# Performance work log

Hardware: AMD Instinct MI355X
Metric: run time of the kernel (lower is better)

The kernel has to match this reference:

```python
import jax, jax.numpy as jnp
import numpy as np

DIM = 1024
STATE = 64
HEADS = 8
EXPAND = 2
INNER = DIM * EXPAND          # 2048
HEAD_DIM = INNER // HEADS     # 256
KERNEL = 4
B, L = 2, 2048
EPS = 1e-5


def setup_inputs() -> dict:
    key = jax.random.key(0)
    ks = jax.random.split(key, 12)
    s = 0.02
    return {
        "input_tensor": jax.random.normal(ks[0], (B, L, DIM), jnp.float32),
        "Wx": jax.random.normal(ks[1], (INNER, DIM), jnp.float32) * s,
        "Wz": jax.random.normal(ks[2], (INNER, DIM), jnp.float32) * s,
        "conv_w": jax.random.normal(ks[3], (INNER, 1, KERNEL), jnp.float32) * s,
        "conv_b": jnp.zeros((INNER,), jnp.float32),
        "Wb": jax.random.normal(ks[4], (HEADS * STATE, INNER), jnp.float32) * s,
        "Wc": jax.random.normal(ks[5], (HEADS * STATE, INNER), jnp.float32) * s,
        "Wdt": jax.random.normal(ks[6], (HEADS, INNER), jnp.float32) * s,
        "b_dt": jnp.zeros((HEADS,), jnp.float32),
        "log_a": jnp.log(jnp.full((HEADS,), 0.5, jnp.float32)),
        "d_param": jnp.ones((HEADS,), jnp.float32),
        "gn_w": jnp.ones((INNER,), jnp.float32),
        "gn_b": jnp.zeros((INNER,), jnp.float32),
        "Wout": jax.random.normal(ks[7], (DIM, INNER), jnp.float32) * s,
    }


def _causal_conv(x, conv_w, conv_b):
    # x: (B, L, INNER); depthwise conv, kernel 4, left-pad 3 (causal)
    x_pad = jnp.pad(x, ((0, 0), (KERNEL - 1, 0), (0, 0)))
    w = conv_w[:, 0, :]  # (INNER, K)
    y = sum(x_pad[:, k:k + x.shape[1], :] * w[:, k] for k in range(KERNEL))
    return y + conv_b


def _ssd_scan(x, b, c, dt, a):
    # x: (B,L,H,P) b,c: (B,L,H,N) dt: (B,L,H) a: (H,)
    state0 = jnp.zeros((x.shape[0], HEADS, STATE, HEAD_DIM), x.dtype)

    def step(state, inp):
        x_t, b_t, c_t, dt_t = inp  # (B,H,P),(B,H,N),(B,H,N),(B,H)
        decay = jnp.exp(dt_t * a)[..., None, None]          # (B,H,1,1)
        b_bar = (dt_t[..., None] * b_t)                      # (B,H,N)
        state = decay * state + b_bar[..., None] * x_t[:, :, None, :]
        y_t = jnp.einsum("bhn,bhnp->bhp", c_t, state)
        return state, y_t

    xs = (x.transpose(1, 0, 2, 3), b.transpose(1, 0, 2, 3),
          c.transpose(1, 0, 2, 3), dt.transpose(1, 0, 2))
    _, ys = jax.lax.scan(step, state0, xs)  # ys: (L,B,H,P)
    return ys.transpose(1, 0, 2, 3)


def reference(input_tensor, Wx, Wz, conv_w, conv_b, Wb, Wc, Wdt, b_dt,
              log_a, d_param, gn_w, gn_b, Wout):
    bsz, seq, _ = input_tensor.shape
    x = input_tensor @ Wx.T               # (B,L,INNER)
    z = input_tensor @ Wz.T
    x = _causal_conv(x, conv_w, conv_b)
    x = jax.nn.silu(x)
    b = (x @ Wb.T).reshape(bsz, seq, HEADS, STATE)
    c = (x @ Wc.T).reshape(bsz, seq, HEADS, STATE)
    dt = jax.nn.softplus(x @ Wdt.T + b_dt)  # (B,L,H)
    xh = x.reshape(bsz, seq, HEADS, HEAD_DIM)
    a = -jnp.exp(log_a)
    y = _ssd_scan(xh, b, c, dt, a)
    y = y + d_param[None, None, :, None] * xh
    # GroupNorm(HEADS, INNER) applied on (B, C, L): normalize per (batch, group)
    # over (channels-in-group, sequence)
    yg = y  # (B, L, H, P) -- groups are contiguous channel blocks = heads
    mean = yg.mean(axis=(1, 3), keepdims=True)
    var = yg.var(axis=(1, 3), keepdims=True)
    yn = (yg - mean) / jnp.sqrt(var + EPS)
    yn = yn * gn_w.reshape(1, 1, HEADS, HEAD_DIM) + gn_b.reshape(1, 1, HEADS, HEAD_DIM)
    yn = yn.reshape(bsz, seq, INNER)
    out = yn * jax.nn.silu(z)
    return out @ Wout.T
```

## Files before the change

kernel.cpp:

```cpp
#include <hip/hip_runtime.h>
#include <math.h>

#define DIM_   1024
#define STATE_ 64
#define HEADS_ 8
#define INNER_ 2048
#define HDIM_  256
#define B_     2
#define L_     2048
#define M_     (B_*L_)
#define EPS_   1e-5f
#define Q_     64
#define NC_    (L_/Q_)
#define NCHUNK_ (B_*HEADS_*NC_)
#define BCS_   1024
#define XZS_   4096

typedef _Float16 f16;
typedef __attribute__((ext_vector_type(8))) _Float16 half8;
typedef __attribute__((ext_vector_type(4))) _Float16 half4;
typedef __attribute__((ext_vector_type(4))) float    f32x4;

__device__ __forceinline__ float siluf(float x) { return x / (1.f + expf(-x)); }

__device__ __forceinline__ void gload_lds16(const void* g, void* l) {
    __builtin_amdgcn_global_load_lds((const __attribute__((address_space(1))) void*)g,
                                     (__attribute__((address_space(3))) void*)l, 16, 0, 0);
}

__global__ __launch_bounds__(256) void cast_all(const float* __restrict__ in0,
                                                const float* __restrict__ Wx,
                                                const float* __restrict__ Wz,
                                                const float* __restrict__ Wb,
                                                const float* __restrict__ Wc,
                                                const float* __restrict__ Wout,
                                                f16* __restrict__ input_h,
                                                f16* __restrict__ wxz_h,
                                                f16* __restrict__ wbc_h,
                                                f16* __restrict__ wout_h) {
    int i = blockIdx.x * 256 + threadIdx.x;
    const float* src; f16* dst; int off;
    if      (i < 1048576) { src = in0;  dst = input_h;            off = i; }
    else if (i < 1572864) { src = Wx;   dst = wxz_h;              off = i - 1048576; }
    else if (i < 2097152) { src = Wz;   dst = wxz_h + 2097152;    off = i - 1572864; }
    else if (i < 2359296) { src = Wb;   dst = wbc_h;              off = i - 2097152; }
    else if (i < 2621440) { src = Wc;   dst = wbc_h + 1048576;    off = i - 2359296; }
    else                  { src = Wout; dst = wout_h;             off = i - 2621440; }
    float4 v = *(const float4*)&src[(size_t)off * 4];
    half4 o;
    o[0] = (f16)v.x; o[1] = (f16)v.y; o[2] = (f16)v.z; o[3] = (f16)v.w;
    *(half4*)&dst[(size_t)off * 4] = o;
}

template<int BN, bool OUTF16>
__global__ __launch_bounds__(256) void hgemm(const f16* __restrict__ A,
                                             const f16* __restrict__ W,
                                             void* __restrict__ Cout,
                                             int K, int N) {
    constexpr int N_FR = BN / 32;
    constexpr int NITER = (128 + BN) / 64;
    __shared__ f16 sA[128 * 32];
    __shared__ f16 sW[BN * 32];
    const int tid  = threadIdx.x;
    const int wid  = tid >> 6;
    const int lane = tid & 63;
    const int bm = blockIdx.y * 128;
    const int bn = blockIdx.x * BN;
    const int wr = wid >> 1, wc = wid & 1;
    const int r  = lane & 15, kg = lane >> 4;

    const f16* gsrc[NITER];
    f16* ldst[NITER];
#pragma unroll
    for (int i = 0; i < NITER; ++i) {
        int slot = tid + i * 256;
        if (slot < 512) {
            int row = slot >> 2;
            int kgv = ((slot & 3) ^ ((row >> 1) & 3)) * 8;
            gsrc[i] = A + (size_t)(bm + row) * K + kgv;
        } else {
            int row = (slot - 512) >> 2;
            int kgv = ((slot & 3) ^ ((row >> 1) & 3)) * 8;
            gsrc[i] = W + (size_t)(bn + row) * K + kgv;
        }
        int slot0 = (tid & ~63) + i * 256;
        ldst[i] = (slot0 < 512) ? &sA[slot0 * 8] : &sW[(slot0 - 512) * 8];
    }

    int aoff[4], boff[N_FR];
#pragma unroll
    for (int m = 0; m < 4; ++m) {
        int arow = wr * 64 + m * 16 + r;
        aoff[m] = arow * 32 + ((kg ^ ((arow >> 1) & 3)) << 3);
    }
#pragma unroll
    for (int n = 0; n < N_FR; ++n) {
        int wrow = wc * (BN / 2) + n * 16 + r;
        boff[n] = wrow * 32 + ((kg ^ ((wrow >> 1) & 3)) << 3);
    }

    f32x4 acc[4][N_FR];
#pragma unroll
    for (int m = 0; m < 4; ++m)
#pragma unroll
        for (int n = 0; n < N_FR; ++n) acc[m][n] = (f32x4)0.f;

    for (int k0 = 0; k0 < K; k0 += 32) {
#pragma unroll
        for (int i = 0; i < NITER; ++i) gload_lds16(gsrc[i] + k0, ldst[i]);
        __syncthreads();
        half8 av[4], bv[N_FR];
#pragma unroll
        for (int m = 0; m < 4; ++m) av[m] = *(const half8*)&sA[aoff[m]];
#pragma unroll
        for (int n = 0; n < N_FR; ++n) bv[n] = *(const half8*)&sW[boff[n]];
#pragma unroll
        for (int m = 0; m < 4; ++m)
#pragma unroll
            for (int n = 0; n < N_FR; ++n)
                acc[m][n] = __builtin_amdgcn_mfma_f32_16x16x32_f16(av[m], bv[n], acc[m][n], 0, 0, 0);
        __syncthreads();
    }

#pragma unroll
    for (int m = 0; m < 4; ++m)
#pragma unroll
        for (int n = 0; n < N_FR; ++n) {
            int row0o = bm + wr * 64 + m * 16 + kg * 4;
            int col   = bn + wc * (BN / 2) + n * 16 + r;
#pragma unroll
            for (int j = 0; j < 4; ++j) {
                if (OUTF16) ((f16*)Cout)[(size_t)(row0o + j) * N + col] = (f16)acc[m][n][j];
                else        ((float*)Cout)[(size_t)(row0o + j) * N + col] = acc[m][n][j];
            }
        }
}

__global__ __launch_bounds__(256) void conv_silu_dt(const f16* __restrict__ xz,
                                                    const float* __restrict__ cw,
                                                    const float* __restrict__ cb,
                                                    const float* __restrict__ Wdt,
                                                    const float* __restrict__ bdt,
                                                    f16* __restrict__ xc,
                                                    float* __restrict__ dtb) {
    __shared__ float sred[4][HEADS_];
    const int m = blockIdx.x;
    const int tid = threadIdx.x;
    const int c8 = tid * 8;
    const int t = m & (L_ - 1);
    float acc[8];
    float4 wv[8];
#pragma unroll
    for (int j = 0; j < 8; ++j) { acc[j] = cb[c8 + j]; wv[j] = *(const float4*)&cw[(c8 + j) * 4]; }
#pragma unroll
    for (int k = 0; k < 4; ++k) {
        int tt = t - 3 + k;
        if (tt >= 0) {
            half8 xv = *(const half8*)&xz[(size_t)(m - 3 + k) * XZS_ + c8];
#pragma unroll
            for (int j = 0; j < 8; ++j) acc[j] += (float)xv[j] * ((const float*)&wv[j])[k];
        }
    }
    float xf[8];
    half8 o;
#pragma unroll
    for (int j = 0; j < 8; ++j) { xf[j] = siluf(acc[j]); o[j] = (f16)xf[j]; }
    *(half8*)&xc[(size_t)m * INNER_ + c8] = o;

    float p[HEADS_];
#pragma unroll
    for (int h = 0; h < HEADS_; ++h) {
        float4 w0 = *(const float4*)&Wdt[h * INNER_ + c8];
        float4 w1 = *(const float4*)&Wdt[h * INNER_ + c8 + 4];
        p[h] = xf[0]*w0.x + xf[1]*w0.y + xf[2]*w0.z + xf[3]*w0.w
             + xf[4]*w1.x + xf[5]*w1.y + xf[6]*w1.z + xf[7]*w1.w;
    }
#pragma unroll
    for (int h = 0; h < HEADS_; ++h)
#pragma unroll
        for (int off = 32; off > 0; off >>= 1)
            p[h] += __shfl_down(p[h], off, 64);
    if ((tid & 63) == 0) {
#pragma unroll
        for (int h = 0; h < HEADS_; ++h) sred[tid >> 6][h] = p[h];
    }
    __syncthreads();
    if (tid < 32) {
        float v = sred[tid >> 3][tid & 7];
        v += __shfl_down(v, 16, 32);
        v += __shfl_down(v, 8, 32);
        if (tid < 8) {
            float s = v + bdt[tid];
            dtb[(size_t)m * HEADS_ + tid] = (s > 20.f) ? s : log1pf(expf(s));
        }
    }
}

__global__ __launch_bounds__(256) void ssd_phase1(const float* __restrict__ bc,
                                                  const float* __restrict__ dtb,
                                                  const float* __restrict__ log_a,
                                                  float* __restrict__ pbuf,
                                                  float* __restrict__ eAbuf,
                                                  float* __restrict__ wbuf,
                                                  float* __restrict__ cdecay) {
    __shared__ float sBt[STATE_][Q_+1];
    __shared__ float sCt[STATE_][Q_+1];
    __shared__ float sA[Q_];
    __shared__ float sDt[Q_];
    const int tid = threadIdx.x;
    const int chunk = blockIdx.x;
    const int bh = chunk / NC_;
    const int ck = chunk - bh * NC_;
    const int b = bh >> 3, h = bh & 7;
    const int m0 = b * L_ + ck * Q_;

    if (tid < 64) {
        float dt = dtb[(size_t)(m0 + tid) * HEADS_ + h];
        float a = -expf(log_a[h]);
        float x = dt * a;
#pragma unroll
        for (int off = 1; off < 64; off <<= 1) {
            float v = __shfl_up(x, off, 64);
            if (tid >= off) x += v;
        }
        float Alast = __shfl(x, 63, 64);
        sA[tid] = x;
        sDt[tid] = dt;
        eAbuf[(size_t)(m0 + tid) * HEADS_ + h] = expf(x);
        wbuf[(size_t)chunk * Q_ + tid] = expf(Alast - x) * dt;
        if (tid == 0) cdecay[chunk] = expf(Alast);
    }
#pragma unroll
    for (int l = 0; l < 4; ++l) {
        int q = tid + l * 256;
        int s = q >> 4;
        int n0 = (q & 15) * 4;
        float4 bv = *(const float4*)&bc[(size_t)(m0+s)*BCS_ + h*STATE_ + n0];
        float4 cv = *(const float4*)&bc[(size_t)(m0+s)*BCS_ + 512 + h*STATE_ + n0];
        sBt[n0+0][s] = bv.x; sBt[n0+1][s] = bv.y; sBt[n0+2][s] = bv.z; sBt[n0+3][s] = bv.w;
        sCt[n0+0][s] = cv.x; sCt[n0+1][s] = cv.y; sCt[n0+2][s] = cv.z; sCt[n0+3][s] = cv.w;
    }
    __syncthreads();
    const int tx = tid & 15, ty = tid >> 4;
    float g[4][4];
#pragma unroll
    for (int i = 0; i < 4; ++i)
#pragma unroll
        for (int j = 0; j < 4; ++j) g[i][j] = 0.f;
    for (int n = 0; n < STATE_; ++n) {
        float cv[4], bv[4];
#pragma unroll
        for (int i = 0; i < 4; ++i) cv[i] = sCt[n][ty*4+i];
#pragma unroll
        for (int j = 0; j < 4; ++j) bv[j] = sBt[n][tx*4+j];
#pragma unroll
        for (int i = 0; i < 4; ++i)
#pragma unroll
            for (int j = 0; j < 4; ++j) g[i][j] += cv[i] * bv[j];
    }
#pragma unroll
    for (int i = 0; i < 4; ++i) {
        int t = ty*4 + i;
        float At = sA[t];
        float o[4];
#pragma unroll
        for (int j = 0; j < 4; ++j) {
            int s = tx*4 + j;
            o[j] = (t >= s) ? g[i][j] * expf(At - sA[s]) * sDt[s] : 0.f;
        }
        *(float4*)&pbuf[((size_t)chunk * Q_ + t) * Q_ + tx*4] = make_float4(o[0],o[1],o[2],o[3]);
    }
}

__global__ __launch_bounds__(256) void ssd_phase2(const float* __restrict__ bc,
                                                  const f16* __restrict__ xch,
                                                  const float* __restrict__ pbuf,
                                                  const float* __restrict__ wbuf,
                                                  float* __restrict__ ybuf,
                                                  float* __restrict__ sloc) {
    __shared__ float sPt[Q_][Q_+1];
    __shared__ float sBw[Q_][STATE_+1];
    __shared__ float sX[Q_][Q_+4];
    const int tid = threadIdx.x;
    const int chunk = blockIdx.x;
    const int bh = chunk / NC_;
    const int ck = chunk - bh * NC_;
    const int b = bh >> 3, h = bh & 7;
    const int m0 = b * L_ + ck * Q_;

#pragma unroll
    for (int l = 0; l < 4; ++l) {
        int q = tid + l * 256;
        int t = q >> 4;
        int s0 = (q & 15) * 4;
        float4 pv = *(const float4*)&pbuf[((size_t)chunk*Q_ + t)*Q_ + s0];
        sPt[s0+0][t] = pv.x; sPt[s0+1][t] = pv.y; sPt[s0+2][t] = pv.z; sPt[s0+3][t] = pv.w;
        int s = t;
        int n0 = s0;
        float ws = wbuf[(size_t)chunk * Q_ + s];
        float4 bv = *(const float4*)&bc[(size_t)(m0+s)*BCS_ + h*STATE_ + n0];
        sBw[s][n0+0] = bv.x * ws; sBw[s][n0+1] = bv.y * ws;
        sBw[s][n0+2] = bv.z * ws; sBw[s][n0+3] = bv.w * ws;
    }
    const int tx = tid & 15, ty = tid >> 4;
    for (int pt = 0; pt < 4; ++pt) {
        int p0 = pt * 64;
        __syncthreads();
#pragma unroll
        for (int l = 0; l < 2; ++l) {
            int q = tid + l * 256;
            int s = q >> 3;
            int pp = (q & 7) * 8;
            half8 xv = *(const half8*)&xch[(size_t)(m0+s)*INNER_ + h*HDIM_ + p0 + pp];
#pragma unroll
            for (int j = 0; j < 8; ++j) sX[s][pp+j] = (float)xv[j];
        }
        __syncthreads();
        float accY[4][4], accS[4][4];
#pragma unroll
        for (int i = 0; i < 4; ++i)
#pragma unroll
            for (int j = 0; j < 4; ++j) { accY[i][j] = 0.f; accS[i][j] = 0.f; }
        for (int s = 0; s < Q_; ++s) {
            float pv[4], bv[4];
#pragma unroll
            for (int i = 0; i < 4; ++i) { pv[i] = sPt[s][ty*4+i]; bv[i] = sBw[s][ty*4+i]; }
            float4 xv = *(const float4*)&sX[s][tx*4];
            float xq[4] = {xv.x, xv.y, xv.z, xv.w};
#pragma unroll
            for (int i = 0; i < 4; ++i)
#pragma unroll
                for (int j = 0; j < 4; ++j) {
                    accY[i][j] += pv[i] * xq[j];
                    accS[i][j] += bv[i] * xq[j];
                }
        }
#pragma unroll
        for (int i = 0; i < 4; ++i) {
            int t = ty*4 + i;
            *(float4*)&ybuf[(size_t)(m0+t)*INNER_ + h*HDIM_ + p0 + tx*4] =
                make_float4(accY[i][0], accY[i][1], accY[i][2], accY[i][3]);
            *(float4*)&sloc[((size_t)chunk*STATE_ + t)*HDIM_ + p0 + tx*4] =
                make_float4(accS[i][0], accS[i][1], accS[i][2], accS[i][3]);
        }
    }
}

__global__ __launch_bounds__(256) void chunk_scan_k(float* __restrict__ sloc,
                                                    const float* __restrict__ cdecay) {
    int bh = blockIdx.x >> 6;
    int el = (blockIdx.x & 63) * 256 + threadIdx.x;
    float s = 0.f;
    for (int c = 0; c < NC_; ++c) {
        size_t chunk = (size_t)bh * NC_ + c;
        float* ptr = sloc + chunk * (size_t)(STATE_*HDIM_) + el;
        float tmp = *ptr;
        *ptr = s;
        s = cdecay[chunk] * s + tmp;
    }
}

__global__ __launch_bounds__(256) void ssd_phase3(const float* __restrict__ bc,
                                                  const f16* __restrict__ xch,
                                                  const float* __restrict__ sloc,
                                                  const float* __restrict__ eAbuf,
                                                  const float* __restrict__ dparam,
                                                  float* __restrict__ ybuf,
                                                  float* __restrict__ gstats) {
    __shared__ float sCt[STATE_][Q_+1];
    __shared__ float sS[STATE_][Q_+4];
    __shared__ float red[512];
    const int tid = threadIdx.x;
    const int chunk = blockIdx.x;
    const int bh = chunk / NC_;
    const int ck = chunk - bh * NC_;
    const int b = bh >> 3, h = bh & 7;
    const int m0 = b * L_ + ck * Q_;

#pragma unroll
    for (int l = 0; l < 4; ++l) {
        int q = tid + l * 256;
        int t = q >> 4;
        int n0 = (q & 15) * 4;
        float4 cv = *(const float4*)&bc[(size_t)(m0+t)*BCS_ + 512 + h*STATE_ + n0];
        sCt[n0+0][t] = cv.x; sCt[n0+1][t] = cv.y; sCt[n0+2][t] = cv.z; sCt[n0+3][t] = cv.w;
    }
    const int tx = tid & 15, ty = tid >> 4;
    const float d = dparam[h];
    float lsum = 0.f, lsq = 0.f;
    for (int pt = 0; pt < 4; ++pt) {
        int p0 = pt * 64;
        __syncthreads();
#pragma unroll
        for (int l = 0; l < 4; ++l) {
            int q = tid + l * 256;
            int n = q >> 4;
            int pp = (q & 15) * 4;
            *(float4*)&sS[n][pp] = *(const float4*)&sloc[((size_t)chunk*STATE_ + n)*HDIM_ + p0 + pp];
        }
        __syncthreads();
        float acc[4][4];
#pragma unroll
        for (int i = 0; i < 4; ++i)
#pragma unroll
            for (int j = 0; j < 4; ++j) acc[i][j] = 0.f;
        for (int n = 0; n < STATE_; ++n) {
            float cv[4];
#pragma unroll
            for (int i = 0; i < 4; ++i) cv[i] = sCt[n][ty*4+i];
            float4 sv = *(const float4*)&sS[n][tx*4];
            float sq[4] = {sv.x, sv.y, sv.z, sv.w};
#pragma unroll
            for (int i = 0; i < 4; ++i)
#pragma unroll
                for (int j = 0; j < 4; ++j) acc[i][j] += cv[i] * sq[j];
        }
#pragma unroll
        for (int i = 0; i < 4; ++i) {
            int t = ty*4 + i;
            float eA = eAbuf[(size_t)(m0+t)*HEADS_ + h];
            size_t off = (size_t)(m0+t)*INNER_ + h*HDIM_ + p0 + tx*4;
            float4 yin = *(const float4*)&ybuf[off];
            half4 xv4 = *(const half4*)&xch[off];
            float4 o;
            o.x = yin.x + eA*acc[i][0] + d*(float)xv4[0];
            o.y = yin.y + eA*acc[i][1] + d*(float)xv4[1];
            o.z = yin.z + eA*acc[i][2] + d*(float)xv4[2];
            o.w = yin.w + eA*acc[i][3] + d*(float)xv4[3];
            *(float4*)&ybuf[off] = o;
            lsum += o.x + o.y + o.z + o.w;
            lsq  += o.x*o.x + o.y*o.y + o.z*o.z + o.w*o.w;
        }
    }
    __syncthreads();
    red[tid] = lsum; red[256+tid] = lsq;
    __syncthreads();
    for (int st = 128; st > 0; st >>= 1) {
        if (tid < st) { red[tid] += red[tid+st]; red[256+tid] += red[256+tid+st]; }
        __syncthreads();
    }
    if (tid == 0) {
        atomicAdd(&gstats[bh*2+0], red[0]);
        atomicAdd(&gstats[bh*2+1], red[256]);
    }
}

__global__ __launch_bounds__(256) void gn_gate_h(const float* __restrict__ ybuf,
                                                 const f16* __restrict__ xz,
                                                 const float* __restrict__ gstats,
                                                 const float* __restrict__ gnw,
                                                 const float* __restrict__ gnb,
                                                 f16* __restrict__ g) {
    int idx = blockIdx.x * 256 + threadIdx.x;
    int c8 = (idx & (INNER_/8 - 1)) * 8;
    int m = idx >> 8;
    int bh = (m >> 11) * HEADS_ + (c8 >> 8);
    const float cnt = (float)(L_ * HDIM_);
    float mean = gstats[bh*2] / cnt;
    float var  = gstats[bh*2+1] / cnt - mean*mean;
    float rstd = rsqrtf(var + EPS_);
    size_t off = (size_t)m * INNER_ + c8;
    float4 y0 = *(const float4*)&ybuf[off];
    float4 y1 = *(const float4*)&ybuf[off + 4];
    half8 zv = *(const half8*)&xz[(size_t)m * XZS_ + INNER_ + c8];
    float4 w0 = *(const float4*)&gnw[c8], w1 = *(const float4*)&gnw[c8+4];
    float4 b0 = *(const float4*)&gnb[c8], b1 = *(const float4*)&gnb[c8+4];
    float yn[8] = {y0.x, y0.y, y0.z, y0.w, y1.x, y1.y, y1.z, y1.w};
    float wv[8] = {w0.x, w0.y, w0.z, w0.w, w1.x, w1.y, w1.z, w1.w};
    float bv[8] = {b0.x, b0.y, b0.z, b0.w, b1.x, b1.y, b1.z, b1.w};
    half8 o;
#pragma unroll
    for (int j = 0; j < 8; ++j) {
        float v = (yn[j] - mean) * rstd * wv[j] + bv[j];
        o[j] = (f16)(v * siluf((float)zv[j]));
    }
    *(half8*)&g[off] = o;
}

extern "C" void kernel_launch(void* const* d_in, const int* in_sizes, int n_in,
                              void* d_out, int out_size, void* d_ws, size_t ws_size,
                              hipStream_t stream) {
    const float* input  = (const float*)d_in[0];
    const float* Wx     = (const float*)d_in[1];
    const float* Wz     = (const float*)d_in[2];
    const float* conv_w = (const float*)d_in[3];
    const float* conv_b = (const float*)d_in[4];
    const float* Wb     = (const float*)d_in[5];
    const float* Wc     = (const float*)d_in[6];
    const float* Wdt    = (const float*)d_in[7];
    const float* b_dt   = (const float*)d_in[8];
    const float* log_a  = (const float*)d_in[9];
    const float* d_par  = (const float*)d_in[10];
    const float* gn_w   = (const float*)d_in[11];
    const float* gn_b   = (const float*)d_in[12];
    const float* Wout   = (const float*)d_in[13];
    float* out = (float*)d_out;

    float* ws = (float*)d_ws;
    size_t off = 0;
    auto alloc = [&](size_t nfloats) { float* p = ws + off; off += (nfloats + 63) & ~(size_t)63; return p; };
    f16* input_h = (f16*)alloc((size_t)M_*DIM_/2);
    f16* wxz_h   = (f16*)alloc((size_t)XZS_*DIM_/2);
    f16* wbc_h   = (f16*)alloc((size_t)BCS_*INNER_/2);
    f16* wout_h  = (f16*)alloc((size_t)DIM_*INNER_/2);
    f16* xz_h    = (f16*)alloc((size_t)M_*XZS_/2);
    f16* xconv_h = (f16*)alloc((size_t)M_*INNER_/2);
    f16* gbuf_h  = (f16*)alloc((size_t)M_*INNER_/2);
    float* bcmat = alloc((size_t)M_*BCS_);
    float* dtb   = alloc((size_t)M_*HEADS_);
    float* eAb   = alloc((size_t)M_*HEADS_);
    float* wbuf  = alloc((size_t)NCHUNK_*Q_);
    float* ybuf  = alloc((size_t)M_*INNER_);
    float* pbuf  = alloc((size_t)NCHUNK_*Q_*Q_);
    float* sloc  = alloc((size_t)NCHUNK_*STATE_*HDIM_);
    float* cdec  = alloc((size_t)NCHUNK_);
    float* gstat = alloc((size_t)2*B_*HEADS_);

    dim3 blk(256);

    cast_all<<<12288, blk, 0, stream>>>(input, Wx, Wz, Wb, Wc, Wout,
                                        input_h, wxz_h, wbc_h, wout_h);
    hgemm<128,true><<<dim3(XZS_/128, M_/128), blk, 0, stream>>>(input_h, wxz_h, xz_h, DIM_, XZS_);
    conv_silu_dt<<<M_, blk, 0, stream>>>(xz_h, conv_w, conv_b, Wdt, b_dt, xconv_h, dtb);
    hgemm<64,false><<<dim3(BCS_/64, M_/128), blk, 0, stream>>>(xconv_h, wbc_h, bcmat, INNER_, BCS_);
    ssd_phase1<<<NCHUNK_, blk, 0, stream>>>(bcmat, dtb, log_a, pbuf, eAb, wbuf, cdec);
    ssd_phase2<<<NCHUNK_, blk, 0, stream>>>(bcmat, xconv_h, pbuf, wbuf, ybuf, sloc);
    chunk_scan_k<<<B_*HEADS_*64, blk, 0, stream>>>(sloc, cdec);
    hipMemsetAsync(gstat, 0, 2*B_*HEADS_*sizeof(float), stream);
    ssd_phase3<<<NCHUNK_, blk, 0, stream>>>(bcmat, xconv_h, sloc, eAb, d_par, ybuf, gstat);
    gn_gate_h<<<(M_*(INNER_/8))/256, blk, 0, stream>>>(ybuf, xz_h, gstat, gn_w, gn_b, gbuf_h);
    hgemm<64,false><<<dim3(DIM_/64, M_/128), blk, 0, stream>>>(gbuf_h, wout_h, out, INNER_, DIM_);
}
```

Measured before the change: 405.2 us.

## Move chunked SSD scan matmuls onto fp16 MFMA with transposed operands

Result: faster. 363.3 us (-10.4%).

```diff
diff --git a/kernel.cpp b/kernel.cpp
--- a/kernel.cpp
+++ b/kernel.cpp
@@ -196,15 +196,44 @@
     }
 }
 
-__global__ __launch_bounds__(256) void ssd_phase1(const float* __restrict__ bc,
+__global__ __launch_bounds__(256) void xpose_k(const f16* __restrict__ xc,
+                                               f16* __restrict__ xT) {
+    __shared__ f16 sT[64][72];
+    const int blk = blockIdx.x;
+    const int bh = blk >> 7;
+    const int rem = blk & 127;
+    const int tt = rem >> 2;
+    const int pt = rem & 3;
+    const int b = bh >> 3, h = bh & 7;
+    const int tid = threadIdx.x;
+#pragma unroll
+    for (int it = 0; it < 2; ++it) {
+        int q = tid + it * 256;
+        int tr = q >> 3;
+        int p0 = (q & 7) * 8;
+        half8 v = *(const half8*)&xc[(size_t)(b * L_ + tt * 64 + tr) * INNER_ + h * HDIM_ + pt * 64 + p0];
+        *(half8*)&sT[tr][p0] = v;
+    }
+    __syncthreads();
+#pragma unroll
+    for (int it = 0; it < 2; ++it) {
+        int q = tid + it * 256;
+        int pr = q >> 3;
+        int t0 = (q & 7) * 8;
+        half8 v;
+#pragma unroll
+        for (int j = 0; j < 8; ++j) v[j] = sT[t0 + j][pr];
+        *(half8*)&xT[((size_t)bh * HDIM_ + pt * 64 + pr) * L_ + tt * 64 + t0] = v;
+    }
+}
+
+__global__ __launch_bounds__(256) void ssd_phase1(const f16* __restrict__ bc,
                                                   const float* __restrict__ dtb,
                                                   const float* __restrict__ log_a,
-                                                  float* __restrict__ pbuf,
+                                                  f16* __restrict__ pbuf,
                                                   float* __restrict__ eAbuf,
                                                   float* __restrict__ wbuf,
                                                   float* __restrict__ cdecay) {
-    __shared__ float sBt[STATE_][Q_+1];
-    __shared__ float sCt[STATE_][Q_+1];
     __shared__ float sA[Q_];
     __shared__ float sDt[Q_];
     const int tid = threadIdx.x;
@@ -230,145 +259,137 @@
         wbuf[(size_t)chunk * Q_ + tid] = expf(Alast - x) * dt;
         if (tid == 0) cdecay[chunk] = expf(Alast);
     }
-#pragma unroll
-    for (int l = 0; l < 4; ++l) {
-        int q = tid + l * 256;
-        int s = q >> 4;
-        int n0 = (q & 15) * 4;
-        float4 bv = *(const float4*)&bc[(size_t)(m0+s)*BCS_ + h*STATE_ + n0];
-        float4 cv = *(const float4*)&bc[(size_t)(m0+s)*BCS_ + 512 + h*STATE_ + n0];
-        sBt[n0+0][s] = bv.x; sBt[n0+1][s] = bv.y; sBt[n0+2][s] = bv.z; sBt[n0+3][s] = bv.w;
-        sCt[n0+0][s] = cv.x; sCt[n0+1][s] = cv.y; sCt[n0+2][s] = cv.z; sCt[n0+3][s] = cv.w;
-    }
     __syncthreads();
-    const int tx = tid & 15, ty = tid >> 4;
-    float g[4][4];
-#pragma unroll
-    for (int i = 0; i < 4; ++i)
-#pragma unroll
-        for (int j = 0; j < 4; ++j) g[i][j] = 0.f;
-    for (int n = 0; n < STATE_; ++n) {
-        float cv[4], bv[4];
-#pragma unroll
-        for (int i = 0; i < 4; ++i) cv[i] = sCt[n][ty*4+i];
-#pragma unroll
-        for (int j = 0; j < 4; ++j) bv[j] = sBt[n][tx*4+j];
-#pragma unroll
-        for (int i = 0; i < 4; ++i)
-#pragma unroll
-            for (int j = 0; j < 4; ++j) g[i][j] += cv[i] * bv[j];
-    }
-#pragma unroll
-    for (int i = 0; i < 4; ++i) {
-        int t = ty*4 + i;
-        float At = sA[t];
-        float o[4];
+
+    const int w = tid >> 6, lane = tid & 63;
+    const int r = lane & 15, kg = lane >> 4;
+    const int ft = w;
+    const f16* Crow = bc + (size_t)(m0 + ft * 16 + r) * BCS_ + 512 + h * STATE_;
+    half8 a0 = *(const half8*)(Crow + kg * 8);
+    half8 a1 = *(const half8*)(Crow + 32 + kg * 8);
+#pragma unroll
+    for (int fs = 0; fs < 4; ++fs) {
+        const f16* Brow = bc + (size_t)(m0 + fs * 16 + r) * BCS_ + h * STATE_;
+        half8 b0 = *(const half8*)(Brow + kg * 8);
+        half8 b1 = *(const half8*)(Brow + 32 + kg * 8);
+        f32x4 g = (f32x4)0.f;
+        g = __builtin_amdgcn_mfma_f32_16x16x32_f16(a0, b0, g, 0, 0, 0);
+        g = __builtin_amdgcn_mfma_f32_16x16x32_f16(a1, b1, g, 0, 0, 0);
+        int s = fs * 16 + r;
+        float As = sA[s], dts = sDt[s];
 #pragma unroll
         for (int j = 0; j < 4; ++j) {
-            int s = tx*4 + j;
-            o[j] = (t >= s) ? g[i][j] * expf(At - sA[s]) * sDt[s] : 0.f;
-        }
-        *(float4*)&pbuf[((size_t)chunk * Q_ + t) * Q_ + tx*4] = make_float4(o[0],o[1],o[2],o[3]);
-    }
-}
-
-__global__ __launch_bounds__(256) void ssd_phase2(const float* __restrict__ bc,
-                                                  const f16* __restrict__ xch,
-                                                  const float* __restrict__ pbuf,
-                                                  const float* __restrict__ wbuf,
-                                                  float* __restrict__ ybuf,
-                                                  float* __restrict__ sloc) {
-    __shared__ float sPt[Q_][Q_+1];
-    __shared__ float sBw[Q_][STATE_+1];
-    __shared__ float sX[Q_][Q_+4];
-    const int tid = threadIdx.x;
+            int t = ft * 16 + kg * 4 + j;
+            float val = (t >= s) ? g[j] * expf(sA[t] - As) * dts : 0.f;
+            pbuf[((size_t)chunk * Q_ + t) * Q_ + s] = (f16)val;
+        }
+    }
+}
+
+__global__ __launch_bounds__(256) void bwt_k(const f16* __restrict__ bc,
+                                             const float* __restrict__ wbuf,
+                                             f16* __restrict__ bwT) {
+    __shared__ f16 sT[64][72];
+    __shared__ float sw[64];
     const int chunk = blockIdx.x;
     const int bh = chunk / NC_;
     const int ck = chunk - bh * NC_;
     const int b = bh >> 3, h = bh & 7;
     const int m0 = b * L_ + ck * Q_;
-
-#pragma unroll
-    for (int l = 0; l < 4; ++l) {
-        int q = tid + l * 256;
-        int t = q >> 4;
-        int s0 = (q & 15) * 4;
-        float4 pv = *(const float4*)&pbuf[((size_t)chunk*Q_ + t)*Q_ + s0];
-        sPt[s0+0][t] = pv.x; sPt[s0+1][t] = pv.y; sPt[s0+2][t] = pv.z; sPt[s0+3][t] = pv.w;
-        int s = t;
-        int n0 = s0;
-        float ws = wbuf[(size_t)chunk * Q_ + s];
-        float4 bv = *(const float4*)&bc[(size_t)(m0+s)*BCS_ + h*STATE_ + n0];
-        sBw[s][n0+0] = bv.x * ws; sBw[s][n0+1] = bv.y * ws;
-        sBw[s][n0+2] = bv.z * ws; sBw[s][n0+3] = bv.w * ws;
-    }
-    const int tx = tid & 15, ty = tid >> 4;
-    for (int pt = 0; pt < 4; ++pt) {
-        int p0 = pt * 64;
-        __syncthreads();
-#pragma unroll
-        for (int l = 0; l < 2; ++l) {
-            int q = tid + l * 256;
-            int s = q >> 3;
-            int pp = (q & 7) * 8;
-            half8 xv = *(const half8*)&xch[(size_t)(m0+s)*INNER_ + h*HDIM_ + p0 + pp];
-#pragma unroll
-            for (int j = 0; j < 8; ++j) sX[s][pp+j] = (float)xv[j];
-        }
-        __syncthreads();
-        float accY[4][4], accS[4][4];
-#pragma unroll
-        for (int i = 0; i < 4; ++i)
-#pragma unroll
-            for (int j = 0; j < 4; ++j) { accY[i][j] = 0.f; accS[i][j] = 0.f; }
-        for (int s = 0; s < Q_; ++s) {
-            float pv[4], bv[4];
-#pragma unroll
-            for (int i = 0; i < 4; ++i) { pv[i] = sPt[s][ty*4+i]; bv[i] = sBw[s][ty*4+i]; }
-            float4 xv = *(const float4*)&sX[s][tx*4];
-            float xq[4] = {xv.x, xv.y, xv.z, xv.w};
-#pragma unroll
-            for (int i = 0; i < 4; ++i)
-#pragma unroll
-                for (int j = 0; j < 4; ++j) {
-                    accY[i][j] += pv[i] * xq[j];
-                    accS[i][j] += bv[i] * xq[j];
-                }
-        }
-#pragma unroll
-        for (int i = 0; i < 4; ++i) {
-            int t = ty*4 + i;
-            *(float4*)&ybuf[(size_t)(m0+t)*INNER_ + h*HDIM_ + p0 + tx*4] =
-                make_float4(accY[i][0], accY[i][1], accY[i][2], accY[i][3]);
-            *(float4*)&sloc[((size_t)chunk*STATE_ + t)*HDIM_ + p0 + tx*4] =
-                make_float4(accS[i][0], accS[i][1], accS[i][2], accS[i][3]);
-        }
-    }
-}
-
-__global__ __launch_bounds__(256) void chunk_scan_k(float* __restrict__ sloc,
+    const int tid = threadIdx.x;
+    if (tid < 64) sw[tid] = wbuf[(size_t)chunk * Q_ + tid];
+#pragma unroll
+    for (int it = 0; it < 2; ++it) {
+        int q = tid + it * 256;
+        int s = q >> 3;
+        int n0 = (q & 7) * 8;
+        half8 v = *(const half8*)&bc[(size_t)(m0 + s) * BCS_ + h * STATE_ + n0];
+        *(half8*)&sT[s][n0] = v;
+    }
+    __syncthreads();
+#pragma unroll
+    for (int it = 0; it < 2; ++it) {
+        int q = tid + it * 256;
+        int n = q >> 3;
+        int s0 = (q & 7) * 8;
+        half8 o;
+#pragma unroll
+        for (int j = 0; j < 8; ++j) o[j] = (f16)((float)sT[s0 + j][n] * sw[s0 + j]);
+        *(half8*)&bwT[((size_t)chunk * Q_ + n) * Q_ + s0] = o;
+    }
+}
+
+__global__ __launch_bounds__(256) void ssd_phase2(const f16* __restrict__ xT,
+                                                  const f16* __restrict__ bwT,
+                                                  f16* __restrict__ sloc) {
+    const int tid = threadIdx.x;
+    const int chunk = blockIdx.x;
+    const int bh = chunk / NC_;
+    const int ck = chunk - bh * NC_;
+    const int w = tid >> 6, lane = tid & 63;
+    const int r = lane & 15, kg = lane >> 4;
+
+    f32x4 acc[4][4];
+#pragma unroll
+    for (int i = 0; i < 4; ++i)
+#pragma unroll
+        for (int j = 0; j < 4; ++j) acc[i][j] = (f32x4)0.f;
+
+#pragma unroll
+    for (int kk = 0; kk < 2; ++kk) {
+        half8 a[4], bfr[4];
+#pragma unroll
+        for (int pf = 0; pf < 4; ++pf) {
+            int p = w * 64 + pf * 16 + r;
+            a[pf] = *(const half8*)&xT[((size_t)bh * HDIM_ + p) * L_ + ck * Q_ + kk * 32 + kg * 8];
+        }
+#pragma unroll
+        for (int nf = 0; nf < 4; ++nf) {
+            int n = nf * 16 + r;
+            bfr[nf] = *(const half8*)&bwT[((size_t)chunk * Q_ + n) * Q_ + kk * 32 + kg * 8];
+        }
+#pragma unroll
+        for (int pf = 0; pf < 4; ++pf)
+#pragma unroll
+            for (int nf = 0; nf < 4; ++nf)
+                acc[pf][nf] = __builtin_amdgcn_mfma_f32_16x16x32_f16(a[pf], bfr[nf], acc[pf][nf], 0, 0, 0);
+    }
+#pragma unroll
+    for (int pf = 0; pf < 4; ++pf)
+#pragma unroll
+        for (int nf = 0; nf < 4; ++nf) {
+            int n = nf * 16 + r;
+#pragma unroll
+            for (int j = 0; j < 4; ++j) {
+                int p = w * 64 + pf * 16 + kg * 4 + j;
+                sloc[((size_t)chunk * HDIM_ + p) * STATE_ + n] = (f16)acc[pf][nf][j];
+            }
+        }
+}
+
+__global__ __launch_bounds__(256) void chunk_scan_k(f16* __restrict__ sloc,
                                                     const float* __restrict__ cdecay) {
     int bh = blockIdx.x >> 6;
     int el = (blockIdx.x & 63) * 256 + threadIdx.x;
     float s = 0.f;
     for (int c = 0; c < NC_; ++c) {
         size_t chunk = (size_t)bh * NC_ + c;
-        float* ptr = sloc + chunk * (size_t)(STATE_*HDIM_) + el;
-        float tmp = *ptr;
-        *ptr = s;
+        f16* ptr = sloc + chunk * (size_t)(STATE_*HDIM_) + el;
+        float tmp = (float)*ptr;
+        *ptr = (f16)s;
         s = cdecay[chunk] * s + tmp;
     }
 }
 
-__global__ __launch_bounds__(256) void ssd_phase3(const float* __restrict__ bc,
+__global__ __launch_bounds__(256) void ssd_phase3(const f16* __restrict__ bc,
+                                                  const f16* __restrict__ pbuf,
+                                                  const f16* __restrict__ xT,
+                                                  const f16* __restrict__ sloc,
                                                   const f16* __restrict__ xch,
-                                                  const float* __restrict__ sloc,
                                                   const float* __restrict__ eAbuf,
                                                   const float* __restrict__ dparam,
-                                                  float* __restrict__ ybuf,
+                                                  f16* __restrict__ ybuf,
                                                   float* __restrict__ gstats) {
-    __shared__ float sCt[STATE_][Q_+1];
-    __shared__ float sS[STATE_][Q_+4];
     __shared__ float red[512];
     const int tid = threadIdx.x;
     const int chunk = blockIdx.x;
@@ -376,76 +397,81 @@
     const int ck = chunk - bh * NC_;
     const int b = bh >> 3, h = bh & 7;
     const int m0 = b * L_ + ck * Q_;
-
-#pragma unroll
-    for (int l = 0; l < 4; ++l) {
-        int q = tid + l * 256;
-        int t = q >> 4;
-        int n0 = (q & 15) * 4;
-        float4 cv = *(const float4*)&bc[(size_t)(m0+t)*BCS_ + 512 + h*STATE_ + n0];
-        sCt[n0+0][t] = cv.x; sCt[n0+1][t] = cv.y; sCt[n0+2][t] = cv.z; sCt[n0+3][t] = cv.w;
-    }
-    const int tx = tid & 15, ty = tid >> 4;
+    const int w = tid >> 6, lane = tid & 63;
+    const int r = lane & 15, kg = lane >> 4;
+
+    float eA[4];
+#pragma unroll
+    for (int ft = 0; ft < 4; ++ft)
+        eA[ft] = eAbuf[(size_t)(m0 + ft * 16 + r) * HEADS_ + h];
+
+    f32x4 acc[4][4];
+#pragma unroll
+    for (int i = 0; i < 4; ++i)
+#pragma unroll
+        for (int j = 0; j < 4; ++j) acc[i][j] = (f32x4)0.f;
+
+#pragma unroll
+    for (int ks = 0; ks < 4; ++ks) {
+        half8 a[4], bfr[4];
+#pragma unroll
+        for (int ft = 0; ft < 4; ++ft) {
+            int t = ft * 16 + r;
+            if (ks < 2) {
+                a[ft] = *(const half8*)&pbuf[((size_t)chunk * Q_ + t) * Q_ + ks * 32 + kg * 8];
+            } else {
+                half8 c = *(const half8*)&bc[(size_t)(m0 + t) * BCS_ + 512 + h * STATE_ + (ks - 2) * 32 + kg * 8];
+                half8 sc;
+#pragma unroll
+                for (int j = 0; j < 8; ++j) sc[j] = (f16)(eA[ft] * (float)c[j]);
+                a[ft] = sc;
+            }
+        }
+#pragma unroll
+        for (int pf = 0; pf < 4; ++pf) {
+            int p = w * 64 + pf * 16 + r;
+            if (ks < 2)
+                bfr[pf] = *(const half8*)&xT[((size_t)bh * HDIM_ + p) * L_ + ck * Q_ + ks * 32 + kg * 8];
+            else
+                bfr[pf] = *(const half8*)&sloc[((size_t)chunk * HDIM_ + p) * STATE_ + (ks - 2) * 32 + kg * 8];
+        }
+#pragma unroll
+        for (int ft = 0; ft < 4; ++ft)
+#pragma unroll
+            for (int pf = 0; pf < 4; ++pf)
+                acc[ft][pf] = __builtin_amdgcn_mfma_f32_16x16x32_f16(a[ft], bfr[pf], acc[ft][pf], 0, 0, 0);
+    }
+
     const float d = dparam[h];
     float lsum = 0.f, lsq = 0.f;
-    for (int pt = 0; pt < 4; ++pt) {
-        int p0 = pt * 64;
-        __syncthreads();
-#pragma unroll
-        for (int l = 0; l < 4; ++l) {
-            int q = tid + l * 256;
-            int n = q >> 4;
-            int pp = (q & 15) * 4;
-            *(float4*)&sS[n][pp] = *(const float4*)&sloc[((size_t)chunk*STATE_ + n)*HDIM_ + p0 + pp];
-        }
-        __syncthreads();
-        float acc[4][4];
-#pragma unroll
-        for (int i = 0; i < 4; ++i)
-#pragma unroll
-            for (int j = 0; j < 4; ++j) acc[i][j] = 0.f;
-        for (int n = 0; n < STATE_; ++n) {
-            float cv[4];
-#pragma unroll
-            for (int i = 0; i < 4; ++i) cv[i] = sCt[n][ty*4+i];
-            float4 sv = *(const float4*)&sS[n][tx*4];
-            float sq[4] = {sv.x, sv.y, sv.z, sv.w};
-#pragma unroll
-            for (int i = 0; i < 4; ++i)
-#pragma unroll
-                for (int j = 0; j < 4; ++j) acc[i][j] += cv[i] * sq[j];
-        }
-#pragma unroll
-        for (int i = 0; i < 4; ++i) {
-            int t = ty*4 + i;
-            float eA = eAbuf[(size_t)(m0+t)*HEADS_ + h];
-            size_t off = (size_t)(m0+t)*INNER_ + h*HDIM_ + p0 + tx*4;
-            float4 yin = *(const float4*)&ybuf[off];
-            half4 xv4 = *(const half4*)&xch[off];
-            float4 o;
-            o.x = yin.x + eA*acc[i][0] + d*(float)xv4[0];
-            o.y = yin.y + eA*acc[i][1] + d*(float)xv4[1];
-            o.z = yin.z + eA*acc[i][2] + d*(float)xv4[2];
-            o.w = yin.w + eA*acc[i][3] + d*(float)xv4[3];
-            *(float4*)&ybuf[off] = o;
-            lsum += o.x + o.y + o.z + o.w;
-            lsq  += o.x*o.x + o.y*o.y + o.z*o.z + o.w*o.w;
-        }
-    }
+#pragma unroll
+    for (int ft = 0; ft < 4; ++ft)
+#pragma unroll
+        for (int pf = 0; pf < 4; ++pf) {
+            int p = w * 64 + pf * 16 + r;
+#pragma unroll
+            for (int j = 0; j < 4; ++j) {
+                int t = ft * 16 + kg * 4 + j;
+                size_t off = (size_t)(m0 + t) * INNER_ + h * HDIM_ + p;
+                float y = acc[ft][pf][j] + d * (float)xch[off];
+                ybuf[off] = (f16)y;
+                lsum += y; lsq += y * y;
+            }
+        }
     __syncthreads();
-    red[tid] = lsum; red[256+tid] = lsq;
+    red[tid] = lsum; red[256 + tid] = lsq;
     __syncthreads();
     for (int st = 128; st > 0; st >>= 1) {
-        if (tid < st) { red[tid] += red[tid+st]; red[256+tid] += red[256+tid+st]; }
+        if (tid < st) { red[tid] += red[tid + st]; red[256 + tid] += red[256 + tid + st]; }
         __syncthreads();
     }
     if (tid == 0) {
-        atomicAdd(&gstats[bh*2+0], red[0]);
-        atomicAdd(&gstats[bh*2+1], red[256]);
-    }
-}
-
-__global__ __launch_bounds__(256) void gn_gate_h(const float* __restrict__ ybuf,
+        atomicAdd(&gstats[bh * 2 + 0], red[0]);
+        atomicAdd(&gstats[bh * 2 + 1], red[256]);
+    }
+}
+
+__global__ __launch_bounds__(256) void gn_gate_h(const f16* __restrict__ ybuf,
                                                  const f16* __restrict__ xz,
                                                  const float* __restrict__ gstats,
                                                  const float* __restrict__ gnw,
@@ -460,18 +486,16 @@
     float var  = gstats[bh*2+1] / cnt - mean*mean;
     float rstd = rsqrtf(var + EPS_);
     size_t off = (size_t)m * INNER_ + c8;
-    float4 y0 = *(const float4*)&ybuf[off];
-    float4 y1 = *(const float4*)&ybuf[off + 4];
+    half8 yv = *(const half8*)&ybuf[off];
     half8 zv = *(const half8*)&xz[(size_t)m * XZS_ + INNER_ + c8];
     float4 w0 = *(const float4*)&gnw[c8], w1 = *(const float4*)&gnw[c8+4];
     float4 b0 = *(const float4*)&gnb[c8], b1 = *(const float4*)&gnb[c8+4];
-    float yn[8] = {y0.x, y0.y, y0.z, y0.w, y1.x, y1.y, y1.z, y1.w};
     float wv[8] = {w0.x, w0.y, w0.z, w0.w, w1.x, w1.y, w1.z, w1.w};
     float bv[8] = {b0.x, b0.y, b0.z, b0.w, b1.x, b1.y, b1.z, b1.w};
     half8 o;
 #pragma unroll
     for (int j = 0; j < 8; ++j) {
-        float v = (yn[j] - mean) * rstd * wv[j] + bv[j];
+        float v = ((float)yv[j] - mean) * rstd * wv[j] + bv[j];
         o[j] = (f16)(v * siluf((float)zv[j]));
     }
     *(half8*)&g[off] = o;
@@ -505,14 +529,16 @@
     f16* wout_h  = (f16*)alloc((size_t)DIM_*INNER_/2);
     f16* xz_h    = (f16*)alloc((size_t)M_*XZS_/2);
     f16* xconv_h = (f16*)alloc((size_t)M_*INNER_/2);
+    f16* xT_h    = (f16*)alloc((size_t)M_*INNER_/2);
     f16* gbuf_h  = (f16*)alloc((size_t)M_*INNER_/2);
-    float* bcmat = alloc((size_t)M_*BCS_);
+    f16* bcmat_h = (f16*)alloc((size_t)M_*BCS_/2);
+    f16* pbuf_h  = (f16*)alloc((size_t)NCHUNK_*Q_*Q_/2);
+    f16* bwT_h   = (f16*)alloc((size_t)NCHUNK_*Q_*Q_/2);
+    f16* sloc_h  = (f16*)alloc((size_t)NCHUNK_*STATE_*HDIM_/2);
+    f16* ybuf_h  = (f16*)alloc((size_t)M_*INNER_/2);
     float* dtb   = alloc((size_t)M_*HEADS_);
     float* eAb   = alloc((size_t)M_*HEADS_);
     float* wbuf  = alloc((size_t)NCHUNK_*Q_);
-    float* ybuf  = alloc((size_t)M_*INNER_);
-    float* pbuf  = alloc((size_t)NCHUNK_*Q_*Q_);
-    float* sloc  = alloc((size_t)NCHUNK_*STATE_*HDIM_);
     float* cdec  = alloc((size_t)NCHUNK_);
     float* gstat = alloc((size_t)2*B_*HEADS_);
 
@@ -522,12 +548,15 @@
                                         input_h, wxz_h, wbc_h, wout_h);
     hgemm<128,true><<<dim3(XZS_/128, M_/128), blk, 0, stream>>>(input_h, wxz_h, xz_h, DIM_, XZS_);
     conv_silu_dt<<<M_, blk, 0, stream>>>(xz_h, conv_w, conv_b, Wdt, b_dt, xconv_h, dtb);
-    hgemm<64,false><<<dim3(BCS_/64, M_/128), blk, 0, stream>>>(xconv_h, wbc_h, bcmat, INNER_, BCS_);
-    ssd_phase1<<<NCHUNK_, blk, 0, stream>>>(bcmat, dtb, log_a, pbuf, eAb, wbuf, cdec);
-    ssd_phase2<<<NCHUNK_, blk, 0, stream>>>(bcmat, xconv_h, pbuf, wbuf, ybuf, sloc);
-    chunk_scan_k<<<B_*HEADS_*64, blk, 0, stream>>>(sloc, cdec);
+    hgemm<64,true><<<dim3(BCS_/64, M_/128), blk, 0, stream>>>(xconv_h, wbc_h, bcmat_h, INNER_, BCS_);
+    xpose_k<<<2048, blk, 0, stream>>>(xconv_h, xT_h);
+    ssd_phase1<<<NCHUNK_, blk, 0, stream>>>(bcmat_h, dtb, log_a, pbuf_h, eAb, wbuf, cdec);
+    bwt_k<<<NCHUNK_, blk, 0, stream>>>(bcmat_h, wbuf, bwT_h);
+    ssd_phase2<<<NCHUNK_, blk, 0, stream>>>(xT_h, bwT_h, sloc_h);
+    chunk_scan_k<<<B_*HEADS_*64, blk, 0, stream>>>(sloc_h, cdec);
     hipMemsetAsync(gstat, 0, 2*B_*HEADS_*sizeof(float), stream);
-    ssd_phase3<<<NCHUNK_, blk, 0, stream>>>(bcmat, xconv_h, sloc, eAb, d_par, ybuf, gstat);
-    gn_gate_h<<<(M_*(INNER_/8))/256, blk, 0, stream>>>(ybuf, xz_h, gstat, gn_w, gn_b, gbuf_h);
+    ssd_phase3<<<NCHUNK_, blk, 0, stream>>>(bcmat_h, pbuf_h, xT_h, sloc_h, xconv_h,
+                                            eAb, d_par, ybuf_h, gstat);
+    gn_gate_h<<<(M_*(INNER_/8))/256, blk, 0, stream>>>(ybuf_h, xz_h, gstat, gn_w, gn_b, gbuf_h);
     hgemm<64,false><<<dim3(DIM_/64, M_/128), blk, 0, stream>>>(gbuf_h, wout_h, out, INNER_, DIM_);
 }
```
